# Optimization experiments

Measured on AMD Instinct MI355X. Metric: run time of the kernel, lower is better.

## Reference

```python
import jax, jax.numpy as jnp
import numpy as np

B, T, C, H = 4, 2048, 1024, 16
HD = C // H  # head dim = 64


def setup_inputs() -> dict:
    key = jax.random.key(0)
    ks = jax.random.split(key, 8)
    s = 1.0 / np.sqrt(C)
    return {
        "x": jax.random.normal(ks[0], (B, T, C), dtype=jnp.float32),
        "Wq": jax.random.normal(ks[1], (C, C), dtype=jnp.float32) * s,
        "bq": jax.random.normal(ks[2], (C,), dtype=jnp.float32) * 0.02,
        "Wk": jax.random.normal(ks[3], (C, C), dtype=jnp.float32) * s,
        "bk": jax.random.normal(ks[4], (C,), dtype=jnp.float32) * 0.02,
        "Wv": jax.random.normal(ks[5], (C, C), dtype=jnp.float32) * s,
        "bv": jax.random.normal(ks[6], (C,), dtype=jnp.float32) * 0.02,
        "Wp": jax.random.normal(ks[7], (C, C), dtype=jnp.float32) * s,
    }


def reference(x, Wq, bq, Wk, bk, Wv, bv, Wp):
    # Separate Q/K/V projections (torch Linear: y = x @ W.T + b)
    q = jnp.einsum("btc,dc->btd", x, Wq) + bq
    k = jnp.einsum("btc,dc->btd", x, Wk) + bk
    v = jnp.einsum("btc,dc->btd", x, Wv) + bv
    # split heads -> [B, H, T, HD]
    q = q.reshape(B, T, H, HD).transpose(0, 2, 1, 3)
    k = k.reshape(B, T, H, HD).transpose(0, 2, 1, 3)
    v = v.reshape(B, T, H, HD).transpose(0, 2, 1, 3)
    # causal scaled dot-product attention
    scale = 1.0 / np.sqrt(HD)
    scores = jnp.einsum("bhqd,bhkd->bhqk", q, k) * scale
    causal_mask = jnp.tril(jnp.ones((T, T), dtype=bool))  # [T, T]
    scores = jnp.where(causal_mask, scores, jnp.finfo(scores.dtype).min)
    att = jax.nn.softmax(scores, axis=-1)
    y = jnp.einsum("bhqk,bhkd->bhqd", att, v)
    # merge heads and output projection (no bias)
    y = y.transpose(0, 2, 1, 3).reshape(B, T, C)
    return jnp.einsum("btc,dc->btd", y, Wp)
```

## Files before the change

### kernel.cpp

```cpp
#include <hip/hip_runtime.h>
#include <stdint.h>


typedef unsigned short u16;
typedef short bf16x8 __attribute__((ext_vector_type(8)));
typedef float f32x4  __attribute__((ext_vector_type(4)));

#define LOG2E 1.4426950408889634f
#define CSHIFT 8.0f

__device__ __forceinline__ void gload_lds16(const void* g, void* l) {
  __builtin_amdgcn_global_load_lds(
      (const __attribute__((address_space(1))) void*)g,
      (__attribute__((address_space(3))) void*)l,
      16, 0, 0);
}

__device__ __forceinline__ u16 f2bf(float f) {
  union { float f; uint32_t u; } v; v.f = f;
  uint32_t u = v.u;
  u += 0x7fffu + ((u >> 16) & 1u);
  return (u16)(u >> 16);
}

__device__ __forceinline__ uint32_t pack_bf16(float a, float b) {
#if __has_builtin(__builtin_amdgcn_cvt_pk_bf16_f32)
  typedef short v2s __attribute__((ext_vector_type(2)));
  v2s r = __builtin_amdgcn_cvt_pk_bf16_f32(a, b);
  union { v2s s; uint32_t u; } c; c.s = r;
  return c.u;
#else
  return (uint32_t)f2bf(a) | ((uint32_t)f2bf(b) << 16);
#endif
}

__device__ __forceinline__ float fexp2(float x) {
#if __has_builtin(__builtin_amdgcn_exp2f)
  return __builtin_amdgcn_exp2f(x);
#else
  return exp2f(x);
#endif
}

__global__ __launch_bounds__(256) void cvt_tile_kernel(
    const float* __restrict__ x,
    const float* __restrict__ w0, const float* __restrict__ w1,
    const float* __restrict__ w2, const float* __restrict__ w3,
    u16* __restrict__ ws) {
  __shared__ __attribute__((aligned(16))) u16 lds[16][1032];
  const int t = threadIdx.x;
  const int rb = blockIdx.x;
  const float* src;
  u16* dst;
  int tile, r;
  if (rb < 512) {
    src = x; dst = ws; tile = rb >> 3; r = rb & 7;
  } else {
    const int j = rb - 512;
    const int seg = j >> 6, local = j & 63;
    src = (seg == 0) ? w0 : (seg == 1) ? w1 : (seg == 2) ? w2 : w3;
    dst = ws + 8388608 + (size_t)seg * 1048576;
    tile = local >> 3; r = local & 7;
  }
  const int row0 = tile * 128 + r * 16;

#pragma unroll
  for (int p2 = 0; p2 < 16; ++p2) {
    const float4 v = *(const float4*)(src + (size_t)(row0 + p2) * 1024 + t * 4);
    uint2 pk;
    pk.x = pack_bf16(v.x, v.y);
    pk.y = pack_bf16(v.z, v.w);
    *(uint2*)&lds[p2][t * 4] = pk;
  }
  __syncthreads();

  const int wv = t >> 6, ln = t & 63;
  const int lr = ln & 15, lc = (ln >> 4) * 8;
#pragma unroll
  for (int k8 = 0; k8 < 8; ++k8) {
    const int ks = k8 * 4 + wv;
    const uint4 val = *(const uint4*)&lds[lr][ks * 32 + lc];
    *(uint4*)(dst + ((((size_t)tile * 32 + ks) * 8 + r) * 64 + ln) * 8) = val;
  }
}

__global__ __launch_bounds__(256, 3) void gemm_qkv(
    const u16* __restrict__ A,
    const u16* __restrict__ Wq, const u16* __restrict__ Wk, const u16* __restrict__ Wv,
    const float* __restrict__ bq, const float* __restrict__ bk, const float* __restrict__ bv,
    u16* __restrict__ Qo, u16* __restrict__ Ko, u16* __restrict__ Vo) {
  __shared__ __attribute__((aligned(16))) u16 shm[24576];
  const int tid = threadIdx.x;
  const int wv = tid >> 6, lane = tid & 63;
  const int cl = lane & 15, quad = lane >> 4;
  const int m0 = blockIdx.x * 128;
  const int mat = blockIdx.y >> 3;
  const int nt0 = blockIdx.y & 7;
  const int n0 = nt0 * 128;
  const int wm = (wv >> 1) * 64, wn = (wv & 1) * 64;
  const u16* W = (mat == 0) ? Wq : (mat == 1) ? Wk : Wv;
  const float* bias = (mat == 0) ? bq : (mat == 1) ? bk : bv;

  const u16* Abase = A + ((size_t)blockIdx.x << 17);
  const u16* Wbase = W + ((size_t)nt0 << 17);

  auto stage = [&](int buf, int ks) {
    const u16* a = Abase + ((size_t)ks << 12);
    const u16* w = Wbase + ((size_t)ks << 12);
    u16* la = &shm[buf * 4096];
    u16* lb = &shm[12288 + buf * 4096];
    gload_lds16(a + tid * 8,        la + tid * 8);
    gload_lds16(a + 2048 + tid * 8, la + 2048 + tid * 8);
    gload_lds16(w + tid * 8,        lb + tid * 8);
    gload_lds16(w + 2048 + tid * 8, lb + 2048 + tid * 8);
  };

  f32x4 acc[4][4] = {};

  stage(0, 0);
  stage(1, 1);

  for (int kt = 0; kt < 32; ++kt) {
    if (kt < 31) {
      asm volatile("s_waitcnt vmcnt(4)" ::: "memory");
    } else {
      asm volatile("s_waitcnt vmcnt(0)" ::: "memory");
    }
    __builtin_amdgcn_s_barrier();
    if (kt < 30) stage((kt + 2) % 3, kt + 2);
    const int buf = kt % 3;
    const u16* la = &shm[buf * 4096];
    const u16* lb = &shm[12288 + buf * 4096];
    bf16x8 af[4], bfr[4];
#pragma unroll
    for (int i = 0; i < 4; i++)
      af[i] = *(const bf16x8*)&la[(((wm >> 4) + i) * 64 + lane) * 8];
#pragma unroll
    for (int j = 0; j < 4; j++)
      bfr[j] = *(const bf16x8*)&lb[(((wn >> 4) + j) * 64 + lane) * 8];
#pragma unroll
    for (int i = 0; i < 4; i++)
#pragma unroll
      for (int j = 0; j < 4; j++)
        acc[i][j] = __builtin_amdgcn_mfma_f32_16x16x32_bf16(af[i], bfr[j], acc[i][j], 0, 0, 0);
  }

  __syncthreads();
  u16* etile = shm;

  if (mat == 2) {
#pragma unroll
    for (int j = 0; j < 4; j++) {
      const int n_loc = wn + j * 16 + cl;
      const float bj = bias[n0 + n_loc];
      const int hh = n_loc >> 6, hd = n_loc & 63;
#pragma unroll
      for (int i = 0; i < 4; i++) {
        const int tb = wm + i * 16 + quad * 4;
        uint2 pk;
        pk.x = pack_bf16(acc[i][j][0] + bj, acc[i][j][1] + bj);
        pk.y = pack_bf16(acc[i][j][2] + bj, acc[i][j][3] + bj);
        const int off = ((hd >> 4) * 4 + ((tb >> 5) & 3)) * 512
                      + (((tb >> 3) & 3) * 16 + (hd & 15)) * 8 + (tb & 7);
        *(uint2*)&etile[hh * 8192 + off] = pk;
      }
    }
  } else if (mat == 1) {
#pragma unroll
    for (int j = 0; j < 4; j++) {
      const int n_loc = wn + j * 16 + cl;
      const float bj = bias[n0 + n_loc];
      const int hh = n_loc >> 6, hd = n_loc & 63;
      const int rlo = hd >> 5, lhi = ((hd >> 3) & 3) * 16, e = hd & 7;
#pragma unroll
      for (int i = 0; i < 4; i++) {
#pragma unroll
        for (int r = 0; r < 4; r++) {
          const int tl = wm + i * 16 + quad * 4 + r;
          const int off = (((tl >> 4) & 7) * 2 + rlo) * 512 + (lhi + (tl & 15)) * 8 + e;
          etile[hh * 8192 + off] = f2bf(acc[i][j][r] + bj);
        }
      }
    }
  } else {
    const float sc = 0.125f * LOG2E;
#pragma unroll
    for (int j = 0; j < 4; j++) {
      const int n_loc = wn + j * 16 + cl;
      const float bj = bias[n0 + n_loc];
      const int hh = n_loc >> 6, hd = n_loc & 63;
#pragma unroll
      for (int i = 0; i < 4; i++) {
#pragma unroll
        for (int r = 0; r < 4; r++) {
          const int tl = wm + i * 16 + quad * 4 + r;
          etile[hh * 8192 + tl * 64 + hd] = f2bf((acc[i][j][r] + bj) * sc);
        }
      }
    }
  }
  __syncthreads();

  const int b = m0 >> 11, t0 = m0 & 2047;
  const int h0 = n0 >> 6;
  if (mat == 0) {
#pragma unroll
    for (int p = 0; p < 8; ++p) {
      const int idx = p * 2048 + tid * 8;
      const int hh = idx >> 13, off = idx & 8191;
      u16* dst = Qo + ((size_t)(b * 16 + h0 + hh) * 2048 + t0) * 64 + off;
      *(uint4*)dst = *(const uint4*)&etile[idx];
    }
  } else {
    u16* base = (mat == 1) ? Ko : Vo;
    const int kt = t0 >> 7;
#pragma unroll
    for (int p = 0; p < 8; ++p) {
      const int idx = p * 2048 + tid * 8;
      const int hh = idx >> 13, off = idx & 8191;
      u16* dst = base + ((size_t)(b * 16 + h0 + hh) << 17) + ((size_t)kt << 13) + off;
      *(uint4*)dst = *(const uint4*)&etile[idx];
    }
  }
}

__global__ __launch_bounds__(256, 3) void gemm_out(
    const u16* __restrict__ A, const u16* __restrict__ W,
    float* __restrict__ out) {
  __shared__ __attribute__((aligned(16))) u16 shm[24576];
  const int tid = threadIdx.x;
  const int wv = tid >> 6, lane = tid & 63;
  const int cl = lane & 15, quad = lane >> 4;
  const int m0 = blockIdx.x * 128;
  const int n0 = blockIdx.y * 128;
  const int wm = (wv >> 1) * 64, wn = (wv & 1) * 64;

  const u16* Abase = A + ((size_t)blockIdx.x << 17);
  const u16* Wbase = W + ((size_t)blockIdx.y << 17);

  auto stage = [&](int buf, int ks) {
    const u16* a = Abase + ((size_t)ks << 12);
    const u16* w = Wbase + ((size_t)ks << 12);
    u16* la = &shm[buf * 4096];
    u16* lb = &shm[12288 + buf * 4096];
    gload_lds16(a + tid * 8,        la + tid * 8);
    gload_lds16(a + 2048 + tid * 8, la + 2048 + tid * 8);
    gload_lds16(w + tid * 8,        lb + tid * 8);
    gload_lds16(w + 2048 + tid * 8, lb + 2048 + tid * 8);
  };

  f32x4 acc[4][4] = {};

  stage(0, 0);
  stage(1, 1);

  for (int kt = 0; kt < 32; ++kt) {
    if (kt < 31) {
      asm volatile("s_waitcnt vmcnt(4)" ::: "memory");
    } else {
      asm volatile("s_waitcnt vmcnt(0)" ::: "memory");
    }
    __builtin_amdgcn_s_barrier();
    if (kt < 30) stage((kt + 2) % 3, kt + 2);
    const int buf = kt % 3;
    const u16* la = &shm[buf * 4096];
    const u16* lb = &shm[12288 + buf * 4096];
    bf16x8 af[4], bfr[4];
#pragma unroll
    for (int i = 0; i < 4; i++)
      af[i] = *(const bf16x8*)&la[(((wm >> 4) + i) * 64 + lane) * 8];
#pragma unroll
    for (int j = 0; j < 4; j++)
      bfr[j] = *(const bf16x8*)&lb[(((wn >> 4) + j) * 64 + lane) * 8];
#pragma unroll
    for (int i = 0; i < 4; i++)
#pragma unroll
      for (int j = 0; j < 4; j++)
        acc[i][j] = __builtin_amdgcn_mfma_f32_16x16x32_bf16(af[i], bfr[j], acc[i][j], 0, 0, 0);
  }

  __syncthreads();
  float* etf = (float*)shm;
#pragma unroll
  for (int p = 0; p < 2; ++p) {
    if ((wm >> 6) == p) {
#pragma unroll
      for (int j = 0; j < 4; j++) {
        const int col = wn + j * 16 + cl;
#pragma unroll
        for (int i = 0; i < 4; i++)
#pragma unroll
          for (int r = 0; r < 4; r++) {
            const int row = i * 16 + quad * 4 + r;
            etf[row * 128 + col] = acc[i][j][r];
          }
      }
    }
    __syncthreads();
#pragma unroll
    for (int c = 0; c < 8; ++c) {
      const int lin4 = c * 256 + tid;
      const int fidx = lin4 * 4;
      const int row = fidx >> 7, col = fidx & 127;
      *(float4*)(out + (size_t)(m0 + p * 64 + row) * 1024 + n0 + col) =
          *(const float4*)&etf[fidx];
    }
    __syncthreads();
  }
}

__global__ __launch_bounds__(256, 2) void attn_kernel(
    const u16* __restrict__ Qb, const u16* __restrict__ Kb,
    const u16* __restrict__ Vtb, u16* __restrict__ Yb) {
  __shared__ __attribute__((aligned(16))) u16 ldsK[2][8192];
  __shared__ __attribute__((aligned(16))) u16 ldsV[8192];
  __shared__ __attribute__((aligned(16))) u16 ldsP[4][32][128];
  const int tid = threadIdx.x;
  const int wv = tid >> 6, lane = tid & 63;
  const int cl = lane & 15, quad = lane >> 4;
  const int p = blockIdx.x + (blockIdx.y << 3);
  const int xcd = p & 7, l = p >> 3;
  const int bh = xcd * 8 + (l & 7);
  const int qtb = l >> 3;
  const int qhi = 15 - qtb, qlo = qtb;
  const u16* Qh = Qb + (size_t)bh * 2048 * 64;
  const u16* Kh = Kb + ((size_t)bh << 17);
  const u16* Vh = Vtb + ((size_t)bh << 17);

  bf16x8 qf[2][2][2];
#pragma unroll
  for (int t = 0; t < 2; ++t) {
    const int q0 = (t == 0 ? qhi : qlo) * 128;
#pragma unroll
    for (int rt = 0; rt < 2; ++rt)
#pragma unroll
      for (int ks = 0; ks < 2; ++ks)
        qf[t][rt][ks] = *(const bf16x8*)&Qh[(size_t)(q0 + wv * 32 + rt * 16 + cl) * 64 + ks * 32 + quad * 8];
  }

  f32x4 o[2][2][4] = {};
  float ls[2][2] = {};

  auto stageK = [&](int buf, int kt) {
    const u16* kb2 = Kh + ((size_t)kt << 13);
#pragma unroll
    for (int rep = 0; rep < 4; ++rep)
      gload_lds16(kb2 + (rep * 256 + tid) * 8, &ldsK[buf][(rep * 256 + tid) * 8]);
  };
  auto stageV = [&](int kt) {
    const u16* vb2 = Vh + ((size_t)kt << 13);
#pragma unroll
    for (int rep = 0; rep < 4; ++rep)
      gload_lds16(vb2 + (rep * 256 + tid) * 8, &ldsV[(rep * 256 + tid) * 8]);
  };

  stageK(0, 0);

  for (int kt = 0; kt <= qhi; ++kt) {
    const int buf = kt & 1;
    const bool dolo = (kt <= qlo);
    __syncthreads();

    stageV(kt);

#pragma unroll
    for (int ct = 0; ct < 8; ++ct) {
      const bf16x8 kf0 = *(const bf16x8*)&ldsK[buf][((ct * 2 + 0) * 64 + lane) * 8];
      const bf16x8 kf1 = *(const bf16x8*)&ldsK[buf][((ct * 2 + 1) * 64 + lane) * 8];
#pragma unroll
      for (int rt = 0; rt < 2; ++rt) {
        f32x4 s = {};
        s = __builtin_amdgcn_mfma_f32_16x16x32_bf16(kf0, qf[0][rt][0], s, 0, 0, 0);
        s = __builtin_amdgcn_mfma_f32_16x16x32_bf16(kf1, qf[0][rt][1], s, 0, 0, 0);
        float pv[4];
#pragma unroll
        for (int r = 0; r < 4; ++r) {
          pv[r] = fexp2(s[r] - CSHIFT);
          if (kt == qhi) {
            if (ct * 16 + quad * 4 + r > wv * 32 + rt * 16 + cl) pv[r] = 0.f;
          }
          ls[0][rt] += pv[r];
        }
        const int rl = rt * 16 + cl;
        const int swch = (2 * ct + (quad >> 1)) ^ (cl & 7);
        uint2 pw;
        pw.x = pack_bf16(pv[0], pv[1]);
        pw.y = pack_bf16(pv[2], pv[3]);
        *(uint2*)&ldsP[wv][rl][(swch << 3) + (quad & 1) * 4] = pw;
      }
    }

    __syncthreads();

    if (kt < qhi) stageK(1 - buf, kt + 1);

#pragma unroll
    for (int ks = 0; ks < 4; ++ks) {
      bf16x8 pf[2];
#pragma unroll
      for (int rt = 0; rt < 2; ++rt)
        pf[rt] = *(const bf16x8*)&ldsP[wv][rt * 16 + cl][(((4 * ks + quad) ^ (cl & 7)) << 3)];
#pragma unroll
      for (int nt = 0; nt < 4; ++nt) {
        const bf16x8 vf = *(const bf16x8*)&ldsV[((nt * 4 + ks) * 64 + lane) * 8];
        o[0][0][nt] = __builtin_amdgcn_mfma_f32_16x16x32_bf16(pf[0], vf, o[0][0][nt], 0, 0, 0);
        o[0][1][nt] = __builtin_amdgcn_mfma_f32_16x16x32_bf16(pf[1], vf, o[0][1][nt], 0, 0, 0);
      }
    }

    if (dolo) {
#pragma unroll
      for (int ct = 0; ct < 8; ++ct) {
        const bf16x8 kf0 = *(const bf16x8*)&ldsK[buf][((ct * 2 + 0) * 64 + lane) * 8];
        const bf16x8 kf1 = *(const bf16x8*)&ldsK[buf][((ct * 2 + 1) * 64 + lane) * 8];
#pragma unroll
        for (int rt = 0; rt < 2; ++rt) {
          f32x4 s = {};
          s = __builtin_amdgcn_mfma_f32_16x16x32_bf16(kf0, qf[1][rt][0], s, 0, 0, 0);
          s = __builtin_amdgcn_mfma_f32_16x16x32_bf16(kf1, qf[1][rt][1], s, 0, 0, 0);
          float pv[4];
#pragma unroll
          for (int r = 0; r < 4; ++r) {
            pv[r] = fexp2(s[r] - CSHIFT);
            if (kt == qlo) {
              if (ct * 16 + quad * 4 + r > wv * 32 + rt * 16 + cl) pv[r] = 0.f;
            }
            ls[1][rt] += pv[r];
          }
          const int rl = rt * 16 + cl;
          const int swch = (2 * ct + (quad >> 1)) ^ (cl & 7);
          uint2 pw;
          pw.x = pack_bf16(pv[0], pv[1]);
          pw.y = pack_bf16(pv[2], pv[3]);
          *(uint2*)&ldsP[wv][rl][(swch << 3) + (quad & 1) * 4] = pw;
        }
      }
#pragma unroll
      for (int ks = 0; ks < 4; ++ks) {
        bf16x8 pf[2];
#pragma unroll
        for (int rt = 0; rt < 2; ++rt)
          pf[rt] = *(const bf16x8*)&ldsP[wv][rt * 16 + cl][(((4 * ks + quad) ^ (cl & 7)) << 3)];
#pragma unroll
        for (int nt = 0; nt < 4; ++nt) {
          const bf16x8 vf = *(const bf16x8*)&ldsV[((nt * 4 + ks) * 64 + lane) * 8];
          o[1][0][nt] = __builtin_amdgcn_mfma_f32_16x16x32_bf16(pf[0], vf, o[1][0][nt], 0, 0, 0);
          o[1][1][nt] = __builtin_amdgcn_mfma_f32_16x16x32_bf16(pf[1], vf, o[1][1][nt], 0, 0, 0);
        }
      }
    }
  }

  const int bb = bh >> 4, h = bh & 15;
#pragma unroll
  for (int t = 0; t < 2; ++t) {
    const int q0 = (t == 0 ? qhi : qlo) * 128;
#pragma unroll
    for (int rt = 0; rt < 2; ++rt) {
      float s = ls[t][rt];
      s += __shfl_xor(s, 16, 64);
      s += __shfl_xor(s, 32, 64);
#pragma unroll
      for (int r = 0; r < 4; ++r) {
        const float inv = 1.0f / __shfl(s, quad * 4 + r, 64);
        const int q = q0 + wv * 32 + rt * 16 + quad * 4 + r;
        const int row = bb * 2048 + q;
#pragma unroll
        for (int nt = 0; nt < 4; ++nt) {
          const int col = h * 64 + nt * 16 + cl;
          const size_t off = ((size_t)((row >> 7) * 32 + (col >> 5)) << 12)
                           + (size_t)((((row >> 4) & 7) * 64 + ((col >> 3) & 3) * 16 + (row & 15)) * 8
                                      + (col & 7));
          Yb[off] = f2bf(o[t][rt][nt][r] * inv);
        }
      }
    }
  }
}

extern "C" void kernel_launch(void* const* d_in, const int* in_sizes, int n_in,
                              void* d_out, int out_size, void* d_ws, size_t ws_size,
                              hipStream_t stream) {
  const float* x  = (const float*)d_in[0];
  const float* Wq = (const float*)d_in[1];
  const float* bq = (const float*)d_in[2];
  const float* Wk = (const float*)d_in[3];
  const float* bk = (const float*)d_in[4];
  const float* Wv = (const float*)d_in[5];
  const float* bv = (const float*)d_in[6];
  const float* Wp = (const float*)d_in[7];

  u16* xb  = (u16*)d_ws;
  u16* wqb = xb  + 8388608;
  u16* wkb = wqb + 1048576;
  u16* wvb = wkb + 1048576;
  u16* wpb = wvb + 1048576;
  u16* Qb  = wpb + 1048576;
  u16* Kb  = Qb  + 8388608;
  u16* Vtb = Kb  + 8388608;
  u16* Yb  = Vtb + 8388608;

  cvt_tile_kernel<<<768, 256, 0, stream>>>(x, Wq, Wk, Wv, Wp, (u16*)d_ws);

  gemm_qkv<<<dim3(64, 24), 256, 0, stream>>>(xb, wqb, wkb, wvb, bq, bk, bv,
                                             Qb, Kb, Vtb);

  attn_kernel<<<dim3(8, 64), 256, 0, stream>>>(Qb, Kb, Vtb, Yb);

  gemm_out<<<dim3(64, 8), 256, 0, stream>>>(Yb, wpb, (float*)d_out);
}
```

Before: 233.4 us.

## Split attention q-tile pair across two independent wave groups, read K/V directly

The attention block grows to 512 threads, and each group of four waves handles one of the paired (high, low) query tiles independently instead of processing both sequentially in one group. K and V fragments are now loaded straight from global memory into registers rather than staged through shared memory, which removes all __syncthreads and the LDS double-buffering. This aims to raise parallelism and cut barrier stalls. In exchange it gives up the K/V sharing between the two tiles, so global or L2 traffic rises, and the two groups carry unequal work.

After: 298.6 us. 27.9% more time.

```diff
diff --git a/kernel.cpp b/kernel.cpp
--- a/kernel.cpp
+++ b/kernel.cpp
@@ -309,170 +309,100 @@
   }
 }
 
-__global__ __launch_bounds__(256, 2) void attn_kernel(
+__global__ __launch_bounds__(512, 4) void attn_kernel(
     const u16* __restrict__ Qb, const u16* __restrict__ Kb,
     const u16* __restrict__ Vtb, u16* __restrict__ Yb) {
-  __shared__ __attribute__((aligned(16))) u16 ldsK[2][8192];
-  __shared__ __attribute__((aligned(16))) u16 ldsV[8192];
-  __shared__ __attribute__((aligned(16))) u16 ldsP[4][32][128];
+  __shared__ __attribute__((aligned(16))) u16 ldsP[8][32][128];
   const int tid = threadIdx.x;
-  const int wv = tid >> 6, lane = tid & 63;
+  const int w = tid >> 6;
+  const int g = w >> 2;
+  const int wv = w & 3;
+  const int lane = tid & 63;
   const int cl = lane & 15, quad = lane >> 4;
   const int p = blockIdx.x + (blockIdx.y << 3);
   const int xcd = p & 7, l = p >> 3;
   const int bh = xcd * 8 + (l & 7);
   const int qtb = l >> 3;
-  const int qhi = 15 - qtb, qlo = qtb;
+  const int qt = (g == 0) ? (15 - qtb) : qtb;
   const u16* Qh = Qb + (size_t)bh * 2048 * 64;
   const u16* Kh = Kb + ((size_t)bh << 17);
   const u16* Vh = Vtb + ((size_t)bh << 17);
 
-  bf16x8 qf[2][2][2];
-#pragma unroll
-  for (int t = 0; t < 2; ++t) {
-    const int q0 = (t == 0 ? qhi : qlo) * 128;
-#pragma unroll
-    for (int rt = 0; rt < 2; ++rt)
-#pragma unroll
-      for (int ks = 0; ks < 2; ++ks)
-        qf[t][rt][ks] = *(const bf16x8*)&Qh[(size_t)(q0 + wv * 32 + rt * 16 + cl) * 64 + ks * 32 + quad * 8];
-  }
-
-  f32x4 o[2][2][4] = {};
-  float ls[2][2] = {};
-
-  auto stageK = [&](int buf, int kt) {
-    const u16* kb2 = Kh + ((size_t)kt << 13);
-#pragma unroll
-    for (int rep = 0; rep < 4; ++rep)
-      gload_lds16(kb2 + (rep * 256 + tid) * 8, &ldsK[buf][(rep * 256 + tid) * 8]);
-  };
-  auto stageV = [&](int kt) {
-    const u16* vb2 = Vh + ((size_t)kt << 13);
-#pragma unroll
-    for (int rep = 0; rep < 4; ++rep)
-      gload_lds16(vb2 + (rep * 256 + tid) * 8, &ldsV[(rep * 256 + tid) * 8]);
-  };
-
-  stageK(0, 0);
-
-  for (int kt = 0; kt <= qhi; ++kt) {
-    const int buf = kt & 1;
-    const bool dolo = (kt <= qlo);
-    __syncthreads();
-
-    stageV(kt);
+  bf16x8 qf[2][2];
+  const int q0 = qt * 128;
+#pragma unroll
+  for (int rt = 0; rt < 2; ++rt)
+#pragma unroll
+    for (int ks = 0; ks < 2; ++ks)
+      qf[rt][ks] = *(const bf16x8*)&Qh[(size_t)(q0 + wv * 32 + rt * 16 + cl) * 64 + ks * 32 + quad * 8];
+
+  f32x4 o[2][4] = {};
+  float ls[2] = {};
+
+  for (int kt = 0; kt <= qt; ++kt) {
+    const u16* kc = Kh + ((size_t)kt << 13);
+    const u16* vc = Vh + ((size_t)kt << 13);
 
 #pragma unroll
     for (int ct = 0; ct < 8; ++ct) {
-      const bf16x8 kf0 = *(const bf16x8*)&ldsK[buf][((ct * 2 + 0) * 64 + lane) * 8];
-      const bf16x8 kf1 = *(const bf16x8*)&ldsK[buf][((ct * 2 + 1) * 64 + lane) * 8];
+      const bf16x8 kf0 = *(const bf16x8*)&kc[((ct * 2 + 0) * 64 + lane) * 8];
+      const bf16x8 kf1 = *(const bf16x8*)&kc[((ct * 2 + 1) * 64 + lane) * 8];
 #pragma unroll
       for (int rt = 0; rt < 2; ++rt) {
         f32x4 s = {};
-        s = __builtin_amdgcn_mfma_f32_16x16x32_bf16(kf0, qf[0][rt][0], s, 0, 0, 0);
-        s = __builtin_amdgcn_mfma_f32_16x16x32_bf16(kf1, qf[0][rt][1], s, 0, 0, 0);
+        s = __builtin_amdgcn_mfma_f32_16x16x32_bf16(kf0, qf[rt][0], s, 0, 0, 0);
+        s = __builtin_amdgcn_mfma_f32_16x16x32_bf16(kf1, qf[rt][1], s, 0, 0, 0);
         float pv[4];
 #pragma unroll
         for (int r = 0; r < 4; ++r) {
           pv[r] = fexp2(s[r] - CSHIFT);
-          if (kt == qhi) {
+          if (kt == qt) {
             if (ct * 16 + quad * 4 + r > wv * 32 + rt * 16 + cl) pv[r] = 0.f;
           }
-          ls[0][rt] += pv[r];
+          ls[rt] += pv[r];
         }
         const int rl = rt * 16 + cl;
         const int swch = (2 * ct + (quad >> 1)) ^ (cl & 7);
         uint2 pw;
         pw.x = pack_bf16(pv[0], pv[1]);
         pw.y = pack_bf16(pv[2], pv[3]);
-        *(uint2*)&ldsP[wv][rl][(swch << 3) + (quad & 1) * 4] = pw;
-      }
-    }
-
-    __syncthreads();
-
-    if (kt < qhi) stageK(1 - buf, kt + 1);
+        *(uint2*)&ldsP[w][rl][(swch << 3) + (quad & 1) * 4] = pw;
+      }
+    }
 
 #pragma unroll
     for (int ks = 0; ks < 4; ++ks) {
       bf16x8 pf[2];
 #pragma unroll
       for (int rt = 0; rt < 2; ++rt)
-        pf[rt] = *(const bf16x8*)&ldsP[wv][rt * 16 + cl][(((4 * ks + quad) ^ (cl & 7)) << 3)];
+        pf[rt] = *(const bf16x8*)&ldsP[w][rt * 16 + cl][(((4 * ks + quad) ^ (cl & 7)) << 3)];
 #pragma unroll
       for (int nt = 0; nt < 4; ++nt) {
-        const bf16x8 vf = *(const bf16x8*)&ldsV[((nt * 4 + ks) * 64 + lane) * 8];
-        o[0][0][nt] = __builtin_amdgcn_mfma_f32_16x16x32_bf16(pf[0], vf, o[0][0][nt], 0, 0, 0);
-        o[0][1][nt] = __builtin_amdgcn_mfma_f32_16x16x32_bf16(pf[1], vf, o[0][1][nt], 0, 0, 0);
-      }
-    }
-
-    if (dolo) {
-#pragma unroll
-      for (int ct = 0; ct < 8; ++ct) {
-        const bf16x8 kf0 = *(const bf16x8*)&ldsK[buf][((ct * 2 + 0) * 64 + lane) * 8];
-        const bf16x8 kf1 = *(const bf16x8*)&ldsK[buf][((ct * 2 + 1) * 64 + lane) * 8];
-#pragma unroll
-        for (int rt = 0; rt < 2; ++rt) {
-          f32x4 s = {};
-          s = __builtin_amdgcn_mfma_f32_16x16x32_bf16(kf0, qf[1][rt][0], s, 0, 0, 0);
-          s = __builtin_amdgcn_mfma_f32_16x16x32_bf16(kf1, qf[1][rt][1], s, 0, 0, 0);
-          float pv[4];
-#pragma unroll
-          for (int r = 0; r < 4; ++r) {
-            pv[r] = fexp2(s[r] - CSHIFT);
-            if (kt == qlo) {
-              if (ct * 16 + quad * 4 + r > wv * 32 + rt * 16 + cl) pv[r] = 0.f;
-            }
-            ls[1][rt] += pv[r];
-          }
-          const int rl = rt * 16 + cl;
-          const int swch = (2 * ct + (quad >> 1)) ^ (cl & 7);
-          uint2 pw;
-          pw.x = pack_bf16(pv[0], pv[1]);
-          pw.y = pack_bf16(pv[2], pv[3]);
-          *(uint2*)&ldsP[wv][rl][(swch << 3) + (quad & 1) * 4] = pw;
-        }
-      }
-#pragma unroll
-      for (int ks = 0; ks < 4; ++ks) {
-        bf16x8 pf[2];
-#pragma unroll
-        for (int rt = 0; rt < 2; ++rt)
-          pf[rt] = *(const bf16x8*)&ldsP[wv][rt * 16 + cl][(((4 * ks + quad) ^ (cl & 7)) << 3)];
-#pragma unroll
-        for (int nt = 0; nt < 4; ++nt) {
-          const bf16x8 vf = *(const bf16x8*)&ldsV[((nt * 4 + ks) * 64 + lane) * 8];
-          o[1][0][nt] = __builtin_amdgcn_mfma_f32_16x16x32_bf16(pf[0], vf, o[1][0][nt], 0, 0, 0);
-          o[1][1][nt] = __builtin_amdgcn_mfma_f32_16x16x32_bf16(pf[1], vf, o[1][1][nt], 0, 0, 0);
-        }
+        const bf16x8 vf = *(const bf16x8*)&vc[((nt * 4 + ks) * 64 + lane) * 8];
+        o[0][nt] = __builtin_amdgcn_mfma_f32_16x16x32_bf16(pf[0], vf, o[0][nt], 0, 0, 0);
+        o[1][nt] = __builtin_amdgcn_mfma_f32_16x16x32_bf16(pf[1], vf, o[1][nt], 0, 0, 0);
       }
     }
   }
 
   const int bb = bh >> 4, h = bh & 15;
 #pragma unroll
-  for (int t = 0; t < 2; ++t) {
-    const int q0 = (t == 0 ? qhi : qlo) * 128;
-#pragma unroll
-    for (int rt = 0; rt < 2; ++rt) {
-      float s = ls[t][rt];
-      s += __shfl_xor(s, 16, 64);
-      s += __shfl_xor(s, 32, 64);
-#pragma unroll
-      for (int r = 0; r < 4; ++r) {
-        const float inv = 1.0f / __shfl(s, quad * 4 + r, 64);
-        const int q = q0 + wv * 32 + rt * 16 + quad * 4 + r;
-        const int row = bb * 2048 + q;
-#pragma unroll
-        for (int nt = 0; nt < 4; ++nt) {
-          const int col = h * 64 + nt * 16 + cl;
-          const size_t off = ((size_t)((row >> 7) * 32 + (col >> 5)) << 12)
-                           + (size_t)((((row >> 4) & 7) * 64 + ((col >> 3) & 3) * 16 + (row & 15)) * 8
-                                      + (col & 7));
-          Yb[off] = f2bf(o[t][rt][nt][r] * inv);
-        }
+  for (int rt = 0; rt < 2; ++rt) {
+    float s = ls[rt];
+    s += __shfl_xor(s, 16, 64);
+    s += __shfl_xor(s, 32, 64);
+#pragma unroll
+    for (int r = 0; r < 4; ++r) {
+      const float inv = 1.0f / __shfl(s, quad * 4 + r, 64);
+      const int q = q0 + wv * 32 + rt * 16 + quad * 4 + r;
+      const int row = bb * 2048 + q;
+#pragma unroll
+      for (int nt = 0; nt < 4; ++nt) {
+        const int col = h * 64 + nt * 16 + cl;
+        const size_t off = ((size_t)((row >> 7) * 32 + (col >> 5)) << 12)
+                         + (size_t)((((row >> 4) & 7) * 64 + ((col >> 3) & 3) * 16 + (row & 15)) * 8
+                                    + (col & 7));
+        Yb[off] = f2bf(o[rt][nt][r] * inv);
       }
     }
   }
@@ -505,7 +435,7 @@
   gemm_qkv<<<dim3(64, 24), 256, 0, stream>>>(xb, wqb, wkb, wvb, bq, bk, bv,
                                              Qb, Kb, Vtb);
 
-  attn_kernel<<<dim3(8, 64), 256, 0, stream>>>(Qb, Kb, Vtb, Yb);
+  attn_kernel<<<dim3(8, 64), 512, 0, stream>>>(Qb, Kb, Vtb, Yb);
 
   gemm_out<<<dim3(64, 8), 256, 0, stream>>>(Yb, wpb, (float*)d_out);
 }
```
